# Optimization experiments

Hardware: AMD Instinct MI355X
Metric: run time of the kernel (lower is better)

## Reference

```python
import jax, jax.numpy as jnp
import numpy as np

N_NODES = 100000
NEG_SLOPE = 0.2


def gat_conv(x, src, dst, W, a_src, a_dst, bias, concat):
    """PyG-style GATConv (eval mode, self-loops assumed already added).
    x: [N, F_in], src/dst: [E] (message flows src -> dst).
    W: [F_in, H*C], a_src/a_dst: [H, C], bias: [H*C] or [C].
    """
    H, C = a_src.shape
    N = x.shape[0]
    h = (x @ W).reshape(N, H, C)                      # [N, H, C]
    alpha_src = jnp.einsum('nhc,hc->nh', h, a_src)    # [N, H]
    alpha_dst = jnp.einsum('nhc,hc->nh', h, a_dst)    # [N, H]
    e = jax.nn.leaky_relu(alpha_src[src] + alpha_dst[dst], NEG_SLOPE)  # [E, H]
    # segment softmax over incoming edges of each dst node
    e_max = jax.ops.segment_max(e, dst, num_segments=N)
    e_exp = jnp.exp(e - e_max[dst])
    denom = jax.ops.segment_sum(e_exp, dst, num_segments=N)
    alpha = e_exp / (denom[dst] + 1e-16)              # [E, H]
    msg = h[src] * alpha[:, :, None]                  # [E, H, C]
    out = jax.ops.segment_sum(msg, dst, num_segments=N)  # [N, H, C]
    out = out.reshape(N, H * C) if concat else out.mean(axis=1)
    return out + bias


def add_self_loops(edge_index, n):
    loop = jnp.arange(n, dtype=edge_index.dtype)
    src = jnp.concatenate([edge_index[0], loop])
    dst = jnp.concatenate([edge_index[1], loop])
    return src, dst


def setup_inputs() -> dict:
    key = jax.random.key(0)
    ks = jax.random.split(key, 10)
    F_in, H1, C1, n_cls = 128, 8, 8, 40
    E = 1600000
    x = jax.random.normal(ks[0], (N_NODES, F_in), dtype=jnp.float32)
    edge_index = jax.random.randint(ks[1], (2, E), 0, N_NODES, dtype=jnp.int64)
    g = lambda k, shp, fan: jax.random.normal(k, shp, dtype=jnp.float32) * (1.0 / np.sqrt(fan))
    return {
        'x': x,
        'edge_index': edge_index,
        'W1': g(ks[2], (F_in, H1 * C1), F_in),
        'a_src1': g(ks[3], (H1, C1), C1),
        'a_dst1': g(ks[4], (H1, C1), C1),
        'b1': jnp.zeros((H1 * C1,), dtype=jnp.float32),
        'W2': g(ks[5], (H1 * C1, n_cls), H1 * C1),
        'a_src2': g(ks[6], (1, n_cls), n_cls),
        'a_dst2': g(ks[7], (1, n_cls), n_cls),
        'b2': jnp.zeros((n_cls,), dtype=jnp.float32),
    }


def reference(x, edge_index, W1, a_src1, a_dst1, b1, W2, a_src2, a_dst2, b2):
    src, dst = add_self_loops(edge_index, N_NODES)
    # dropout(p=0.6) layers are identity in eval mode
    h = gat_conv(x, src, dst, W1, a_src1, a_dst1, b1, concat=True)
    h = jax.nn.relu(h)
    out = gat_conv(h, src, dst, W2, a_src2, a_dst2, b2, concat=True)
    return out
```

## Files before the change

### kernel.cpp

```cpp
#include <hip/hip_runtime.h>
#include <math.h>

constexpr int NN     = 100000;
constexpr int E_BASE = 1600000;
constexpr int E_TOT  = E_BASE + NN;
constexpr int F_IN   = 128;
constexpr int F1     = 64;
constexpr int H1n    = 8;
constexpr int F2     = 40;

constexpr int BSHIFT    = 9;
constexpr int NB        = (NN + 511) >> BSHIFT;
constexpr int BCAP      = 12288;
constexpr int P1_BLOCKS = 256;
constexpr int EPB       = (E_TOT + P1_BLOCKS - 1) / P1_BLOCKS;

__device__ __forceinline__ float lrelu(float v) { return fmaxf(v, 0.2f * v); }

__device__ __forceinline__ unsigned bpack(float a, float b) {
    unsigned ua = __float_as_uint(a) + 0x8000u;
    unsigned ub = __float_as_uint(b) + 0x8000u;
    return (ua >> 16) | (ub & 0xFFFF0000u);
}
__device__ __forceinline__ float blo(unsigned u) { return __uint_as_float(u << 16); }
__device__ __forceinline__ float bhi(unsigned u) { return __uint_as_float(u & 0xFFFF0000u); }

__global__ __launch_bounds__(256) void partition(const int* __restrict__ src,
                                                 const int* __restrict__ dst,
                                                 int* __restrict__ bucket_cnt,
                                                 uint2* __restrict__ store) {
    __shared__ int bins[NB];
    __shared__ int base[NB];
    int t = threadIdx.x;
    for (int i = t; i < NB; i += 256) bins[i] = 0;
    __syncthreads();
    int e0 = blockIdx.x * EPB;
    int e1 = min(e0 + EPB, E_TOT);
    for (int e = e0 + t; e < e1; e += 256) {
        int d = (e < E_BASE) ? dst[e] : (e - E_BASE);
        atomicAdd(&bins[d >> BSHIFT], 1);
    }
    __syncthreads();
    for (int i = t; i < NB; i += 256) {
        base[i] = atomicAdd(&bucket_cnt[i], bins[i]);
        bins[i] = 0;
    }
    __syncthreads();
    for (int e = e0 + t; e < e1; e += 256) {
        int s, d;
        if (e < E_BASE) { s = src[e]; d = dst[e]; }
        else            { s = e - E_BASE; d = s; }
        int b = d >> BSHIFT;
        int p = atomicAdd(&bins[b], 1);
        store[(size_t)b * BCAP + base[b] + p] = make_uint2((unsigned)s, (unsigned)d);
    }
}

__global__ void bucket_scan(const int* __restrict__ bucket_cnt,
                            int* __restrict__ bucket_base,
                            int* __restrict__ row_start) {
    if (threadIdx.x == 0) {
        int run = 0;
#pragma unroll 4
        for (int b = 0; b < NB; ++b) { bucket_base[b] = run; run += bucket_cnt[b]; }
        bucket_base[NB] = run;
        row_start[NN] = run;
    }
}

__global__ __launch_bounds__(256) void bucket_csr(const int* __restrict__ bucket_cnt,
                                                  const int* __restrict__ bucket_base,
                                                  const uint2* __restrict__ store,
                                                  int* __restrict__ row_start,
                                                  int* __restrict__ csr_src) {
    __shared__ int cnt_l[512];
    __shared__ int incl[512];
    __shared__ int cur_l[512];
    int b = blockIdx.x;
    int t = threadIdx.x;
    int cnt = bucket_cnt[b];
    int gbase = bucket_base[b];
    int nlo = b << BSHIFT;
    int nodes = min(512, NN - nlo);
    cnt_l[t] = 0; cnt_l[t + 256] = 0;
    __syncthreads();
    const uint2* sp = store + (size_t)b * BCAP;
    for (int i = t; i < cnt; i += 256)
        atomicAdd(&cnt_l[(int)sp[i].y - nlo], 1);
    __syncthreads();
    if (t < 64) {
        int run = 0;
        for (int c = 0; c < 512; c += 64) {
            int v = cnt_l[c + t];
#pragma unroll
            for (int off = 1; off < 64; off <<= 1) {
                int u = __shfl_up(v, off, 64);
                if (t >= off) v += u;
            }
            incl[c + t] = run + v;
            run = __shfl(run + v, 63, 64);
        }
    }
    __syncthreads();
    for (int j = t; j < 512; j += 256) {
        int start = gbase + incl[j] - cnt_l[j];
        cur_l[j] = start;
        if (j < nodes) row_start[nlo + j] = start;
    }
    __syncthreads();
    for (int i = t; i < cnt; i += 256) {
        uint2 ed = sp[i];
        int p = atomicAdd(&cur_l[(int)ed.y - nlo], 1);
        csr_src[p] = (int)ed.x;
    }
}

__global__ __launch_bounds__(256) void linear1(const float* __restrict__ x,
                                               const float* __restrict__ W1,
                                               const float* __restrict__ a_src,
                                               const float* __restrict__ a_dst,
                                               unsigned* __restrict__ h1b,
                                               float* __restrict__ as1,
                                               float* __restrict__ ad1) {
    __shared__ float xs[64][36];
    __shared__ float ws[32 * 64];
    int t = threadIdx.x;
    int nb = blockIdx.x * 64;
    int ct = t & 15, nt = t >> 4;
    int rs = t >> 3, qs = t & 7;
    float acc[4][4] = {};
    for (int K0 = 0; K0 < F_IN; K0 += 32) {
        int r0 = min(nb + rs, NN - 1);
        int r1 = min(nb + rs + 32, NN - 1);
        float4 v0 = *(const float4*)&x[(size_t)r0 * F_IN + K0 + qs * 4];
        float4 v1 = *(const float4*)&x[(size_t)r1 * F_IN + K0 + qs * 4];
        *(float4*)&xs[rs][qs * 4] = v0;
        *(float4*)&xs[rs + 32][qs * 4] = v1;
        const float4* wsrc = (const float4*)&W1[(size_t)K0 * F1];
        *(float4*)&ws[t * 4] = wsrc[t];
        *(float4*)&ws[1024 + t * 4] = wsrc[256 + t];
        __syncthreads();
#pragma unroll 8
        for (int kk = 0; kk < 32; ++kk) {
            float4 w = *(const float4*)&ws[kk * 64 + ct * 4];
            float x0 = xs[nt * 4 + 0][kk];
            float x1 = xs[nt * 4 + 1][kk];
            float x2 = xs[nt * 4 + 2][kk];
            float x3 = xs[nt * 4 + 3][kk];
            acc[0][0] = fmaf(x0, w.x, acc[0][0]); acc[0][1] = fmaf(x0, w.y, acc[0][1]);
            acc[0][2] = fmaf(x0, w.z, acc[0][2]); acc[0][3] = fmaf(x0, w.w, acc[0][3]);
            acc[1][0] = fmaf(x1, w.x, acc[1][0]); acc[1][1] = fmaf(x1, w.y, acc[1][1]);
            acc[1][2] = fmaf(x1, w.z, acc[1][2]); acc[1][3] = fmaf(x1, w.w, acc[1][3]);
            acc[2][0] = fmaf(x2, w.x, acc[2][0]); acc[2][1] = fmaf(x2, w.y, acc[2][1]);
            acc[2][2] = fmaf(x2, w.z, acc[2][2]); acc[2][3] = fmaf(x2, w.w, acc[2][3]);
            acc[3][0] = fmaf(x3, w.x, acc[3][0]); acc[3][1] = fmaf(x3, w.y, acc[3][1]);
            acc[3][2] = fmaf(x3, w.z, acc[3][2]); acc[3][3] = fmaf(x3, w.w, acc[3][3]);
        }
        __syncthreads();
    }
    float4 as4 = ((const float4*)a_src)[ct];
    float4 ds4 = ((const float4*)a_dst)[ct];
#pragma unroll
    for (int i = 0; i < 4; ++i) {
        int n = nb + nt * 4 + i;
        unsigned u0 = bpack(acc[i][0], acc[i][1]);
        unsigned u1 = bpack(acc[i][2], acc[i][3]);
        float ps = acc[i][0] * as4.x + acc[i][1] * as4.y + acc[i][2] * as4.z + acc[i][3] * as4.w;
        float pd = acc[i][0] * ds4.x + acc[i][1] * ds4.y + acc[i][2] * ds4.z + acc[i][3] * ds4.w;
        ps += __shfl_xor(ps, 1, 64);
        pd += __shfl_xor(pd, 1, 64);
        if (n < NN) {
            *(uint2*)&h1b[(size_t)n * 32 + ct * 2] = make_uint2(u0, u1);
            if (!(ct & 1)) {
                as1[n * H1n + (ct >> 1)] = ps;
                ad1[n * H1n + (ct >> 1)] = pd;
            }
        }
    }
}

__global__ void node_agg1(const int* __restrict__ row_start, const int* __restrict__ csr_src,
                          const float* __restrict__ as1, const float* __restrict__ ad1,
                          const unsigned* __restrict__ h1b, const float* __restrict__ b1,
                          float* __restrict__ out1r) {
    int n = blockIdx.x;
    int lane = threadIdx.x;
    int e8 = lane & 7, hp = lane >> 3;
    int il = lane & 31, q = lane >> 5;
    int hc = il >> 2;
    float adv = ad1[n * H1n + hp];
    int lo = row_start[n], hi = row_start[n + 1];
    float ssum = 0.f, acc0 = 0.f, acc1 = 0.f;
    for (int base = lo; base < hi; base += 8) {
        int idx = base + e8;
        bool valid = idx < hi;
        int s = csr_src[valid ? idx : (hi - 1)];
        float v = lrelu(as1[s * H1n + hp] + adv);
        float p = valid ? __expf(v) : 0.f;
        ssum += p;
#pragma unroll
        for (int j = 0; j < 4; ++j) {
            int e = 2 * j + q;
            int   sb = __shfl(s, e, 64);
            float pb = __shfl(p, (hc << 3) | e, 64);
            unsigned u = h1b[(size_t)sb * 32 + il];
            acc0 = fmaf(pb, blo(u), acc0);
            acc1 = fmaf(pb, bhi(u), acc1);
        }
    }
    ssum += __shfl_xor(ssum, 1, 64);
    ssum += __shfl_xor(ssum, 2, 64);
    ssum += __shfl_xor(ssum, 4, 64);
    float sh = __shfl(ssum, hc << 3, 64);
    float p0 = acc0 + __shfl(acc0, il | 32, 64);
    float p1 = acc1 + __shfl(acc1, il | 32, 64);
    if (lane < 32) {
        float r = 1.f / (sh + 1e-16f);
        float2 bv = ((const float2*)b1)[il];
        float2 o;
        o.x = fmaxf(fmaf(p0, r, bv.x), 0.f);
        o.y = fmaxf(fmaf(p1, r, bv.y), 0.f);
        ((float2*)(out1r + (size_t)n * F1))[il] = o;
    }
}

__global__ __launch_bounds__(256) void linear2(const float* __restrict__ out1r,
                                               const float* __restrict__ W2,
                                               const float* __restrict__ a_src2,
                                               const float* __restrict__ a_dst2,
                                               unsigned* __restrict__ h2b,
                                               float* __restrict__ as2,
                                               float* __restrict__ ad2) {
    __shared__ float xs[128][65];
    __shared__ float ws[64 * 40];
    int t = threadIdx.x;
    int nb = blockIdx.x * 128;
    int colq = t & 15, rr = t >> 4;
#pragma unroll
    for (int i = 0; i < 8; ++i) {
        int r = rr + 16 * i;
        int g = min(nb + r, NN - 1);
        float4 v = *(const float4*)&out1r[(size_t)g * F1 + colq * 4];
        xs[r][colq * 4 + 0] = v.x; xs[r][colq * 4 + 1] = v.y;
        xs[r][colq * 4 + 2] = v.z; xs[r][colq * 4 + 3] = v.w;
    }
#pragma unroll
    for (int i = 0; i < 10; ++i) ws[t + 256 * i] = W2[t + 256 * i];
    __syncthreads();
    int ct = t & 7, nt = t >> 3;
    float acc[4][5] = {};
#pragma unroll 4
    for (int k = 0; k < F1; ++k) {
        float w0 = ws[k * 40 + ct * 5 + 0];
        float w1 = ws[k * 40 + ct * 5 + 1];
        float w2 = ws[k * 40 + ct * 5 + 2];
        float w3 = ws[k * 40 + ct * 5 + 3];
        float w4 = ws[k * 40 + ct * 5 + 4];
#pragma unroll
        for (int i = 0; i < 4; ++i) {
            float xv = xs[nt * 4 + i][k];
            acc[i][0] = fmaf(xv, w0, acc[i][0]);
            acc[i][1] = fmaf(xv, w1, acc[i][1]);
            acc[i][2] = fmaf(xv, w2, acc[i][2]);
            acc[i][3] = fmaf(xv, w3, acc[i][3]);
            acc[i][4] = fmaf(xv, w4, acc[i][4]);
        }
    }
    float aw[5], dw[5];
#pragma unroll
    for (int j = 0; j < 5; ++j) { aw[j] = a_src2[ct * 5 + j]; dw[j] = a_dst2[ct * 5 + j]; }
#pragma unroll
    for (int i = 0; i < 4; ++i) {
        int n = nb + nt * 4 + i;
        float vs = acc[i][0] * aw[0] + acc[i][1] * aw[1] + acc[i][2] * aw[2]
                 + acc[i][3] * aw[3] + acc[i][4] * aw[4];
        float vd = acc[i][0] * dw[0] + acc[i][1] * dw[1] + acc[i][2] * dw[2]
                 + acc[i][3] * dw[3] + acc[i][4] * dw[4];
        vs += __shfl_xor(vs, 1, 64); vs += __shfl_xor(vs, 2, 64); vs += __shfl_xor(vs, 4, 64);
        vd += __shfl_xor(vd, 1, 64); vd += __shfl_xor(vd, 2, 64); vd += __shfl_xor(vd, 4, 64);
        if (n < NN && ct == 0) { as2[n] = vs; ad2[n] = vd; }
    }
    __syncthreads();
#pragma unroll
    for (int i = 0; i < 4; ++i) {
        int r = nt * 4 + i;
#pragma unroll
        for (int j = 0; j < 5; ++j) xs[r][ct * 5 + j] = acc[i][j];
    }
    __syncthreads();
    {
        int r = t >> 1, half = t & 1;
        int n = nb + r;
        if (n < NN) {
            unsigned* dp = h2b + (size_t)n * 20 + half * 10;
#pragma unroll
            for (int k = 0; k < 10; ++k)
                dp[k] = bpack(xs[r][half * 20 + 2 * k], xs[r][half * 20 + 2 * k + 1]);
        }
    }
}

__global__ void node_agg2(const int* __restrict__ row_start, const int* __restrict__ csr_src,
                          const float* __restrict__ as2, const float* __restrict__ ad2,
                          const unsigned* __restrict__ h2b, const float* __restrict__ b2,
                          float* __restrict__ out) {
    int n = blockIdx.x;
    int lane = threadIdx.x;
    int e8 = lane & 7;
    int il = lane & 31, q = lane >> 5;
    bool act = il < 20;
    float adv = ad2[n];
    int lo = row_start[n], hi = row_start[n + 1];
    float ssum = 0.f, acc0 = 0.f, acc1 = 0.f;
    for (int base = lo; base < hi; base += 8) {
        int idx = base + e8;
        bool valid = idx < hi;
        int s = csr_src[valid ? idx : (hi - 1)];
        float v = lrelu(as2[s] + adv);
        float p = valid ? __expf(v) : 0.f;
        ssum += p;
#pragma unroll
        for (int j = 0; j < 4; ++j) {
            int e = 2 * j + q;
            int   sb = __shfl(s, e, 64);
            float pb = __shfl(p, e, 64);
            unsigned u = act ? h2b[(size_t)sb * 20 + il] : 0u;
            acc0 = fmaf(pb, blo(u), acc0);
            acc1 = fmaf(pb, bhi(u), acc1);
        }
    }
    ssum += __shfl_xor(ssum, 1, 64);
    ssum += __shfl_xor(ssum, 2, 64);
    ssum += __shfl_xor(ssum, 4, 64);
    float p0 = acc0 + __shfl(acc0, il | 32, 64);
    float p1 = acc1 + __shfl(acc1, il | 32, 64);
    if (lane < 32 && act) {
        float r = 1.f / (ssum + 1e-16f);
        float2 bv = ((const float2*)b2)[il];
        float2 o;
        o.x = fmaf(p0, r, bv.x);
        o.y = fmaf(p1, r, bv.y);
        ((float2*)(out + (size_t)n * F2))[il] = o;
    }
}

extern "C" void kernel_launch(void* const* d_in, const int* in_sizes, int n_in,
                              void* d_out, int out_size, void* d_ws, size_t ws_size,
                              hipStream_t stream) {
    const float* x      = (const float*)d_in[0];
    const int*   ei     = (const int*)d_in[1];
    const float* W1     = (const float*)d_in[2];
    const float* a_src1 = (const float*)d_in[3];
    const float* a_dst1 = (const float*)d_in[4];
    const float* b1     = (const float*)d_in[5];
    const float* W2     = (const float*)d_in[6];
    const float* a_src2 = (const float*)d_in[7];
    const float* a_dst2 = (const float*)d_in[8];
    const float* b2     = (const float*)d_in[9];
    float* out = (float*)d_out;
    const int* srcp = ei;
    const int* dstp = ei + E_BASE;

    unsigned* h1b       = (unsigned*)d_ws;
    uint2*    store     = (uint2*)(h1b + (size_t)NN * 32);
    float*    as1       = (float*)(store + (size_t)NB * BCAP);
    float*    ad1       = as1 + (size_t)NN * H1n;
    float*    out1r     = ad1 + (size_t)NN * H1n;
    unsigned* h2b       = (unsigned*)(out1r + (size_t)NN * F1);
    float*    as2       = (float*)(h2b + (size_t)NN * 20);
    float*    ad2       = as2 + NN;
    int*      row_start = (int*)(ad2 + NN);
    int*      csr_src   = row_start + (NN + 1);
    int*      bucket_cnt= csr_src + E_TOT;
    int*      bucket_base= bucket_cnt + NB;

    hipMemsetAsync(bucket_cnt, 0, NB * sizeof(int), stream);

    partition<<<P1_BLOCKS, 256, 0, stream>>>(srcp, dstp, bucket_cnt, store);
    bucket_scan<<<1, 64, 0, stream>>>(bucket_cnt, bucket_base, row_start);
    bucket_csr<<<NB, 256, 0, stream>>>(bucket_cnt, bucket_base, store, row_start, csr_src);

    linear1<<<(NN + 63) / 64, 256, 0, stream>>>(x, W1, a_src1, a_dst1, h1b, as1, ad1);
    node_agg1<<<NN, 64, 0, stream>>>(row_start, csr_src, as1, ad1, h1b, b1, out1r);

    linear2<<<(NN + 127) / 128, 256, 0, stream>>>(out1r, W2, a_src2, a_dst2, h2b, as2, ad2);
    node_agg2<<<NN, 64, 0, stream>>>(row_start, csr_src, as2, ad2, h2b, b2, out);
}
```

Before: 218.5 us.

## Pack partition entries into 32 bits and widen gathers to 16-byte loads

The partition store now packs the source index and local destination offset into one 32-bit word instead of a uint2, halving scratch traffic in the CSR build. Both aggregation kernels now gather neighbour features with one uint4 load per lane, so 8 edges are processed per iteration instead of 2 per unrolled step. Cross-lane reductions are done with xor shuffles. Layer 2 features are split into a 16-word array and a 4-word array so rows are 16-byte aligned. The trade-off is more shuffle reductions at the end, and in layer 2 only 5 of 8 lanes per edge are active.

```diff
diff --git a/kernel.cpp b/kernel.cpp
--- a/kernel.cpp
+++ b/kernel.cpp
@@ -28,7 +28,7 @@
 __global__ __launch_bounds__(256) void partition(const int* __restrict__ src,
                                                  const int* __restrict__ dst,
                                                  int* __restrict__ bucket_cnt,
-                                                 uint2* __restrict__ store) {
+                                                 unsigned* __restrict__ store) {
     __shared__ int bins[NB];
     __shared__ int base[NB];
     int t = threadIdx.x;
@@ -52,7 +52,7 @@
         else            { s = e - E_BASE; d = s; }
         int b = d >> BSHIFT;
         int p = atomicAdd(&bins[b], 1);
-        store[(size_t)b * BCAP + base[b] + p] = make_uint2((unsigned)s, (unsigned)d);
+        store[(size_t)b * BCAP + base[b] + p] = ((unsigned)s << 9) | (unsigned)(d & 511);
     }
 }
 
@@ -70,7 +70,7 @@
 
 __global__ __launch_bounds__(256) void bucket_csr(const int* __restrict__ bucket_cnt,
                                                   const int* __restrict__ bucket_base,
-                                                  const uint2* __restrict__ store,
+                                                  const unsigned* __restrict__ store,
                                                   int* __restrict__ row_start,
                                                   int* __restrict__ csr_src) {
     __shared__ int cnt_l[512];
@@ -84,9 +84,9 @@
     int nodes = min(512, NN - nlo);
     cnt_l[t] = 0; cnt_l[t + 256] = 0;
     __syncthreads();
-    const uint2* sp = store + (size_t)b * BCAP;
+    const unsigned* sp = store + (size_t)b * BCAP;
     for (int i = t; i < cnt; i += 256)
-        atomicAdd(&cnt_l[(int)sp[i].y - nlo], 1);
+        atomicAdd(&cnt_l[sp[i] & 511], 1);
     __syncthreads();
     if (t < 64) {
         int run = 0;
@@ -109,9 +109,9 @@
     }
     __syncthreads();
     for (int i = t; i < cnt; i += 256) {
-        uint2 ed = sp[i];
-        int p = atomicAdd(&cur_l[(int)ed.y - nlo], 1);
-        csr_src[p] = (int)ed.x;
+        unsigned ed = sp[i];
+        int p = atomicAdd(&cur_l[ed & 511], 1);
+        csr_src[p] = (int)(ed >> 9);
     }
 }
 
@@ -186,11 +186,12 @@
     int n = blockIdx.x;
     int lane = threadIdx.x;
     int e8 = lane & 7, hp = lane >> 3;
-    int il = lane & 31, q = lane >> 5;
-    int hc = il >> 2;
+    int il8 = lane & 7, es = lane >> 3;
     float adv = ad1[n * H1n + hp];
     int lo = row_start[n], hi = row_start[n + 1];
-    float ssum = 0.f, acc0 = 0.f, acc1 = 0.f;
+    float ssum = 0.f;
+    float acc[8] = {};
+    const uint4* h4 = (const uint4*)h1b;
     for (int base = lo; base < hi; base += 8) {
         int idx = base + e8;
         bool valid = idx < hi;
@@ -198,29 +199,44 @@
         float v = lrelu(as1[s * H1n + hp] + adv);
         float p = valid ? __expf(v) : 0.f;
         ssum += p;
-#pragma unroll
-        for (int j = 0; j < 4; ++j) {
-            int e = 2 * j + q;
-            int   sb = __shfl(s, e, 64);
-            float pb = __shfl(p, (hc << 3) | e, 64);
-            unsigned u = h1b[(size_t)sb * 32 + il];
-            acc0 = fmaf(pb, blo(u), acc0);
-            acc1 = fmaf(pb, bhi(u), acc1);
+        int   sb = __shfl(s, es, 64);
+        float pb = __shfl(p, (il8 << 3) | es, 64);
+        if (base + es < hi) {
+            uint4 u = h4[(size_t)sb * 8 + il8];
+            acc[0] = fmaf(pb, blo(u.x), acc[0]);
+            acc[1] = fmaf(pb, bhi(u.x), acc[1]);
+            acc[2] = fmaf(pb, blo(u.y), acc[2]);
+            acc[3] = fmaf(pb, bhi(u.y), acc[3]);
+            acc[4] = fmaf(pb, blo(u.z), acc[4]);
+            acc[5] = fmaf(pb, bhi(u.z), acc[5]);
+            acc[6] = fmaf(pb, blo(u.w), acc[6]);
+            acc[7] = fmaf(pb, bhi(u.w), acc[7]);
         }
     }
     ssum += __shfl_xor(ssum, 1, 64);
     ssum += __shfl_xor(ssum, 2, 64);
     ssum += __shfl_xor(ssum, 4, 64);
-    float sh = __shfl(ssum, hc << 3, 64);
-    float p0 = acc0 + __shfl(acc0, il | 32, 64);
-    float p1 = acc1 + __shfl(acc1, il | 32, 64);
-    if (lane < 32) {
+#pragma unroll
+    for (int m = 8; m < 64; m <<= 1) {
+#pragma unroll
+        for (int k = 0; k < 8; ++k) acc[k] += __shfl_xor(acc[k], m, 64);
+    }
+    float sh = __shfl(ssum, il8 << 3, 64);
+    if (lane < 8) {
         float r = 1.f / (sh + 1e-16f);
-        float2 bv = ((const float2*)b1)[il];
-        float2 o;
-        o.x = fmaxf(fmaf(p0, r, bv.x), 0.f);
-        o.y = fmaxf(fmaf(p1, r, bv.y), 0.f);
-        ((float2*)(out1r + (size_t)n * F1))[il] = o;
+        const float4* bq = (const float4*)(b1 + il8 * 8);
+        float4 bv0 = bq[0], bv1 = bq[1];
+        float4 o0, o1;
+        o0.x = fmaxf(fmaf(acc[0], r, bv0.x), 0.f);
+        o0.y = fmaxf(fmaf(acc[1], r, bv0.y), 0.f);
+        o0.z = fmaxf(fmaf(acc[2], r, bv0.z), 0.f);
+        o0.w = fmaxf(fmaf(acc[3], r, bv0.w), 0.f);
+        o1.x = fmaxf(fmaf(acc[4], r, bv1.x), 0.f);
+        o1.y = fmaxf(fmaf(acc[5], r, bv1.y), 0.f);
+        o1.z = fmaxf(fmaf(acc[6], r, bv1.z), 0.f);
+        o1.w = fmaxf(fmaf(acc[7], r, bv1.w), 0.f);
+        float4* op = (float4*)(out1r + (size_t)n * F1 + il8 * 8);
+        op[0] = o0; op[1] = o1;
     }
 }
 
@@ -228,7 +244,8 @@
                                                const float* __restrict__ W2,
                                                const float* __restrict__ a_src2,
                                                const float* __restrict__ a_dst2,
-                                               unsigned* __restrict__ h2b,
+                                               unsigned* __restrict__ h2a,
+                                               unsigned* __restrict__ h2c,
                                                float* __restrict__ as2,
                                                float* __restrict__ ad2) {
     __shared__ float xs[128][65];
@@ -292,26 +309,31 @@
         int r = t >> 1, half = t & 1;
         int n = nb + r;
         if (n < NN) {
-            unsigned* dp = h2b + (size_t)n * 20 + half * 10;
-#pragma unroll
-            for (int k = 0; k < 10; ++k)
-                dp[k] = bpack(xs[r][half * 20 + 2 * k], xs[r][half * 20 + 2 * k + 1]);
+#pragma unroll
+            for (int k = 0; k < 10; ++k) {
+                int w = half * 10 + k;
+                unsigned val = bpack(xs[r][2 * w], xs[r][2 * w + 1]);
+                if (w < 16) h2a[(size_t)n * 16 + w] = val;
+                else        h2c[(size_t)n * 4 + (w - 16)] = val;
+            }
         }
     }
 }
 
 __global__ void node_agg2(const int* __restrict__ row_start, const int* __restrict__ csr_src,
                           const float* __restrict__ as2, const float* __restrict__ ad2,
-                          const unsigned* __restrict__ h2b, const float* __restrict__ b2,
-                          float* __restrict__ out) {
+                          const unsigned* __restrict__ h2a, const unsigned* __restrict__ h2c,
+                          const float* __restrict__ b2, float* __restrict__ out) {
     int n = blockIdx.x;
     int lane = threadIdx.x;
     int e8 = lane & 7;
-    int il = lane & 31, q = lane >> 5;
-    bool act = il < 20;
+    int il5 = lane & 7, es = lane >> 3;
     float adv = ad2[n];
     int lo = row_start[n], hi = row_start[n + 1];
-    float ssum = 0.f, acc0 = 0.f, acc1 = 0.f;
+    float ssum = 0.f;
+    float acc[8] = {};
+    const uint4* ha4 = (const uint4*)h2a;
+    const uint4* hc4 = (const uint4*)h2c;
     for (int base = lo; base < hi; base += 8) {
         int idx = base + e8;
         bool valid = idx < hi;
@@ -319,28 +341,43 @@
         float v = lrelu(as2[s] + adv);
         float p = valid ? __expf(v) : 0.f;
         ssum += p;
-#pragma unroll
-        for (int j = 0; j < 4; ++j) {
-            int e = 2 * j + q;
-            int   sb = __shfl(s, e, 64);
-            float pb = __shfl(p, e, 64);
-            unsigned u = act ? h2b[(size_t)sb * 20 + il] : 0u;
-            acc0 = fmaf(pb, blo(u), acc0);
-            acc1 = fmaf(pb, bhi(u), acc1);
+        int   sb = __shfl(s, es, 64);
+        float pb = __shfl(p, es, 64);
+        if (base + es < hi && il5 < 5) {
+            uint4 u = (il5 < 4) ? ha4[(size_t)sb * 4 + il5] : hc4[sb];
+            acc[0] = fmaf(pb, blo(u.x), acc[0]);
+            acc[1] = fmaf(pb, bhi(u.x), acc[1]);
+            acc[2] = fmaf(pb, blo(u.y), acc[2]);
+            acc[3] = fmaf(pb, bhi(u.y), acc[3]);
+            acc[4] = fmaf(pb, blo(u.z), acc[4]);
+            acc[5] = fmaf(pb, bhi(u.z), acc[5]);
+            acc[6] = fmaf(pb, blo(u.w), acc[6]);
+            acc[7] = fmaf(pb, bhi(u.w), acc[7]);
         }
     }
     ssum += __shfl_xor(ssum, 1, 64);
     ssum += __shfl_xor(ssum, 2, 64);
     ssum += __shfl_xor(ssum, 4, 64);
-    float p0 = acc0 + __shfl(acc0, il | 32, 64);
-    float p1 = acc1 + __shfl(acc1, il | 32, 64);
-    if (lane < 32 && act) {
+#pragma unroll
+    for (int m = 8; m < 64; m <<= 1) {
+#pragma unroll
+        for (int k = 0; k < 8; ++k) acc[k] += __shfl_xor(acc[k], m, 64);
+    }
+    if (lane < 5) {
         float r = 1.f / (ssum + 1e-16f);
-        float2 bv = ((const float2*)b2)[il];
-        float2 o;
-        o.x = fmaf(p0, r, bv.x);
-        o.y = fmaf(p1, r, bv.y);
-        ((float2*)(out + (size_t)n * F2))[il] = o;
+        const float4* bq = (const float4*)(b2 + il5 * 8);
+        float4 bv0 = bq[0], bv1 = bq[1];
+        float4 o0, o1;
+        o0.x = fmaf(acc[0], r, bv0.x);
+        o0.y = fmaf(acc[1], r, bv0.y);
+        o0.z = fmaf(acc[2], r, bv0.z);
+        o0.w = fmaf(acc[3], r, bv0.w);
+        o1.x = fmaf(acc[4], r, bv1.x);
+        o1.y = fmaf(acc[5], r, bv1.y);
+        o1.z = fmaf(acc[6], r, bv1.z);
+        o1.w = fmaf(acc[7], r, bv1.w);
+        float4* op = (float4*)(out + (size_t)n * F2 + il5 * 8);
+        op[0] = o0; op[1] = o1;
     }
 }
 
@@ -361,28 +398,29 @@
     const int* srcp = ei;
     const int* dstp = ei + E_BASE;
 
-    unsigned* h1b       = (unsigned*)d_ws;
-    uint2*    store     = (uint2*)(h1b + (size_t)NN * 32);
-    float*    as1       = (float*)(store + (size_t)NB * BCAP);
-    float*    ad1       = as1 + (size_t)NN * H1n;
-    float*    out1r     = ad1 + (size_t)NN * H1n;
-    unsigned* h2b       = (unsigned*)(out1r + (size_t)NN * F1);
-    float*    as2       = (float*)(h2b + (size_t)NN * 20);
-    float*    ad2       = as2 + NN;
-    int*      row_start = (int*)(ad2 + NN);
-    int*      csr_src   = row_start + (NN + 1);
-    int*      bucket_cnt= csr_src + E_TOT;
+    unsigned* h1b        = (unsigned*)d_ws;
+    unsigned* storeu     = h1b + (size_t)NN * 32;
+    float*    as1        = (float*)(storeu + (size_t)NB * BCAP);
+    float*    ad1        = as1 + (size_t)NN * H1n;
+    float*    out1r      = ad1 + (size_t)NN * H1n;
+    unsigned* h2a        = (unsigned*)(out1r + (size_t)NN * F1);
+    unsigned* h2c        = h2a + (size_t)NN * 16;
+    float*    as2        = (float*)(h2c + (size_t)NN * 4);
+    float*    ad2        = as2 + NN;
+    int*      row_start  = (int*)(ad2 + NN);
+    int*      csr_src    = row_start + (NN + 1);
+    int*      bucket_cnt = csr_src + E_TOT;
     int*      bucket_base= bucket_cnt + NB;
 
     hipMemsetAsync(bucket_cnt, 0, NB * sizeof(int), stream);
 
-    partition<<<P1_BLOCKS, 256, 0, stream>>>(srcp, dstp, bucket_cnt, store);
+    partition<<<P1_BLOCKS, 256, 0, stream>>>(srcp, dstp, bucket_cnt, storeu);
     bucket_scan<<<1, 64, 0, stream>>>(bucket_cnt, bucket_base, row_start);
-    bucket_csr<<<NB, 256, 0, stream>>>(bucket_cnt, bucket_base, store, row_start, csr_src);
+    bucket_csr<<<NB, 256, 0, stream>>>(bucket_cnt, bucket_base, storeu, row_start, csr_src);
 
     linear1<<<(NN + 63) / 64, 256, 0, stream>>>(x, W1, a_src1, a_dst1, h1b, as1, ad1);
     node_agg1<<<NN, 64, 0, stream>>>(row_start, csr_src, as1, ad1, h1b, b1, out1r);
 
-    linear2<<<(NN + 127) / 128, 256, 0, stream>>>(out1r, W2, a_src2, a_dst2, h2b, as2, ad2);
-    node_agg2<<<NN, 64, 0, stream>>>(row_start, csr_src, as2, ad2, h2b, b2, out);
-}
+    linear2<<<(NN + 127) / 128, 256, 0, stream>>>(out1r, W2, a_src2, a_dst2, h2a, h2c, as2, ad2);
+    node_agg2<<<NN, 64, 0, stream>>>(row_start, csr_src, as2, ad2, h2a, h2c, b2, out);
+}
```

New measurement: 232.3 us. 1.06x slower.

## Pack edge store into 32-bit words and split layer-2 features into aligned arrays

Applied to the files above, without the earlier changes.

Partition now writes each edge as a single 32-bit word (src shifted left by 9 bits, OR'd with the local dst offset) instead of a uint2, halving the scatter store and the bucket_csr read traffic. Layer-2 bf16 features (20 words per node, 80 B rows) are split into a 64-byte-aligned 16-word array plus a 4-word tail array, so that node_agg2 gathers whole aligned lines. The packing relies on src fitting in 23 bits, which holds for this node count. The split adds a second scattered load per gathered row and extra branches in the gather loop.

```diff
diff --git a/kernel.cpp b/kernel.cpp
--- a/kernel.cpp
+++ b/kernel.cpp
@@ -28,7 +28,7 @@
 __global__ __launch_bounds__(256) void partition(const int* __restrict__ src,
                                                  const int* __restrict__ dst,
                                                  int* __restrict__ bucket_cnt,
-                                                 uint2* __restrict__ store) {
+                                                 unsigned* __restrict__ store) {
     __shared__ int bins[NB];
     __shared__ int base[NB];
     int t = threadIdx.x;
@@ -52,7 +52,7 @@
         else            { s = e - E_BASE; d = s; }
         int b = d >> BSHIFT;
         int p = atomicAdd(&bins[b], 1);
-        store[(size_t)b * BCAP + base[b] + p] = make_uint2((unsigned)s, (unsigned)d);
+        store[(size_t)b * BCAP + base[b] + p] = ((unsigned)s << 9) | (unsigned)(d & 511);
     }
 }
 
@@ -70,7 +70,7 @@
 
 __global__ __launch_bounds__(256) void bucket_csr(const int* __restrict__ bucket_cnt,
                                                   const int* __restrict__ bucket_base,
-                                                  const uint2* __restrict__ store,
+                                                  const unsigned* __restrict__ store,
                                                   int* __restrict__ row_start,
                                                   int* __restrict__ csr_src) {
     __shared__ int cnt_l[512];
@@ -84,9 +84,9 @@
     int nodes = min(512, NN - nlo);
     cnt_l[t] = 0; cnt_l[t + 256] = 0;
     __syncthreads();
-    const uint2* sp = store + (size_t)b * BCAP;
+    const unsigned* sp = store + (size_t)b * BCAP;
     for (int i = t; i < cnt; i += 256)
-        atomicAdd(&cnt_l[(int)sp[i].y - nlo], 1);
+        atomicAdd(&cnt_l[sp[i] & 511], 1);
     __syncthreads();
     if (t < 64) {
         int run = 0;
@@ -109,9 +109,9 @@
     }
     __syncthreads();
     for (int i = t; i < cnt; i += 256) {
-        uint2 ed = sp[i];
-        int p = atomicAdd(&cur_l[(int)ed.y - nlo], 1);
-        csr_src[p] = (int)ed.x;
+        unsigned ed = sp[i];
+        int p = atomicAdd(&cur_l[ed & 511], 1);
+        csr_src[p] = (int)(ed >> 9);
     }
 }
 
@@ -228,7 +228,8 @@
                                                const float* __restrict__ W2,
                                                const float* __restrict__ a_src2,
                                                const float* __restrict__ a_dst2,
-                                               unsigned* __restrict__ h2b,
+                                               unsigned* __restrict__ h2a,
+                                               unsigned* __restrict__ h2c,
                                                float* __restrict__ as2,
                                                float* __restrict__ ad2) {
     __shared__ float xs[128][65];
@@ -292,18 +293,21 @@
         int r = t >> 1, half = t & 1;
         int n = nb + r;
         if (n < NN) {
-            unsigned* dp = h2b + (size_t)n * 20 + half * 10;
-#pragma unroll
-            for (int k = 0; k < 10; ++k)
-                dp[k] = bpack(xs[r][half * 20 + 2 * k], xs[r][half * 20 + 2 * k + 1]);
+#pragma unroll
+            for (int k = 0; k < 10; ++k) {
+                int w = half * 10 + k;
+                unsigned val = bpack(xs[r][2 * w], xs[r][2 * w + 1]);
+                if (w < 16) h2a[(size_t)n * 16 + w] = val;
+                else        h2c[(size_t)n * 4 + (w - 16)] = val;
+            }
         }
     }
 }
 
 __global__ void node_agg2(const int* __restrict__ row_start, const int* __restrict__ csr_src,
                           const float* __restrict__ as2, const float* __restrict__ ad2,
-                          const unsigned* __restrict__ h2b, const float* __restrict__ b2,
-                          float* __restrict__ out) {
+                          const unsigned* __restrict__ h2a, const unsigned* __restrict__ h2c,
+                          const float* __restrict__ b2, float* __restrict__ out) {
     int n = blockIdx.x;
     int lane = threadIdx.x;
     int e8 = lane & 7;
@@ -324,7 +328,9 @@
             int e = 2 * j + q;
             int   sb = __shfl(s, e, 64);
             float pb = __shfl(p, e, 64);
-            unsigned u = act ? h2b[(size_t)sb * 20 + il] : 0u;
+            unsigned u = 0u;
+            if (il < 16)      u = h2a[(size_t)sb * 16 + il];
+            else if (il < 20) u = h2c[(size_t)sb * 4 + (il - 16)];
             acc0 = fmaf(pb, blo(u), acc0);
             acc1 = fmaf(pb, bhi(u), acc1);
         }
@@ -361,28 +367,29 @@
     const int* srcp = ei;
     const int* dstp = ei + E_BASE;
 
-    unsigned* h1b       = (unsigned*)d_ws;
-    uint2*    store     = (uint2*)(h1b + (size_t)NN * 32);
-    float*    as1       = (float*)(store + (size_t)NB * BCAP);
-    float*    ad1       = as1 + (size_t)NN * H1n;
-    float*    out1r     = ad1 + (size_t)NN * H1n;
-    unsigned* h2b       = (unsigned*)(out1r + (size_t)NN * F1);
-    float*    as2       = (float*)(h2b + (size_t)NN * 20);
-    float*    ad2       = as2 + NN;
-    int*      row_start = (int*)(ad2 + NN);
-    int*      csr_src   = row_start + (NN + 1);
-    int*      bucket_cnt= csr_src + E_TOT;
+    unsigned* h1b        = (unsigned*)d_ws;
+    unsigned* storeu     = h1b + (size_t)NN * 32;
+    float*    as1        = (float*)(storeu + (size_t)NB * BCAP);
+    float*    ad1        = as1 + (size_t)NN * H1n;
+    float*    out1r      = ad1 + (size_t)NN * H1n;
+    unsigned* h2a        = (unsigned*)(out1r + (size_t)NN * F1);
+    unsigned* h2c        = h2a + (size_t)NN * 16;
+    float*    as2        = (float*)(h2c + (size_t)NN * 4);
+    float*    ad2        = as2 + NN;
+    int*      row_start  = (int*)(ad2 + NN);
+    int*      csr_src    = row_start + (NN + 1);
+    int*      bucket_cnt = csr_src + E_TOT;
     int*      bucket_base= bucket_cnt + NB;
 
     hipMemsetAsync(bucket_cnt, 0, NB * sizeof(int), stream);
 
-    partition<<<P1_BLOCKS, 256, 0, stream>>>(srcp, dstp, bucket_cnt, store);
+    partition<<<P1_BLOCKS, 256, 0, stream>>>(srcp, dstp, bucket_cnt, storeu);
     bucket_scan<<<1, 64, 0, stream>>>(bucket_cnt, bucket_base, row_start);
-    bucket_csr<<<NB, 256, 0, stream>>>(bucket_cnt, bucket_base, store, row_start, csr_src);
+    bucket_csr<<<NB, 256, 0, stream>>>(bucket_cnt, bucket_base, storeu, row_start, csr_src);
 
     linear1<<<(NN + 63) / 64, 256, 0, stream>>>(x, W1, a_src1, a_dst1, h1b, as1, ad1);
     node_agg1<<<NN, 64, 0, stream>>>(row_start, csr_src, as1, ad1, h1b, b1, out1r);
 
-    linear2<<<(NN + 127) / 128, 256, 0, stream>>>(out1r, W2, a_src2, a_dst2, h2b, as2, ad2);
-    node_agg2<<<NN, 64, 0, stream>>>(row_start, csr_src, as2, ad2, h2b, b2, out);
-}
+    linear2<<<(NN + 127) / 128, 256, 0, stream>>>(out1r, W2, a_src2, a_dst2, h2a, h2c, as2, ad2);
+    node_agg2<<<NN, 64, 0, stream>>>(row_start, csr_src, as2, ad2, h2a, h2c, b2, out);
+}
```

Result: slower. 252.5 us (+15.6%).
